# Optimization experiments

Hardware: AMD Instinct MI355X
Metric: run time of the kernel (lower is better)

Reference implementation:

```python
import jax, jax.numpy as jnp
import numpy as np

E = 8        # n_routed_experts
Z = 4        # zero_expert_num (identity experts)
K = 2        # moe_topk
SCALE = 2.5  # routed_scaling_factor
T, H, I = 8192, 1024, 512


def setup_inputs() -> dict:
    key = jax.random.key(0)
    k0, k1, k2, k3, k4 = jax.random.split(key, 5)
    return {
        "hidden_states": jax.random.normal(k0, (T, H), jnp.float32),
        "router_w": jax.random.normal(k1, (E + Z, H), jnp.float32) * 0.02,
        "correction_bias": jax.random.normal(k2, (E + Z,), jnp.float32) * 0.01,
        "w13": jax.random.normal(k3, (E, 2 * I, H), jnp.float32) * 0.02,
        "w2": jax.random.normal(k4, (E, H, I), jnp.float32) * 0.02,
    }


def reference(hidden_states, router_w, correction_bias, w13, w2):
    # ---- router (float32) ----
    logits = hidden_states.astype(jnp.float32) @ router_w.T          # [T, E+Z]
    scores = jax.nn.softmax(logits, axis=-1)
    # correction bias only affects expert *selection*, not the gate weights
    _, topk_idx = jax.lax.top_k(scores + correction_bias, K)          # [T, K]
    topk_w = jnp.take_along_axis(scores, topk_idx, axis=-1)          # renormalize=False

    # ---- zero experts (identity type): idx >= E contributes scale * x ----
    is_zero = topk_idx >= E                                           # [T, K]
    routed_w = jnp.where(is_zero, 0.0, topk_w)
    zero_scale = jnp.where(is_zero, topk_w, 0.0).sum(-1, keepdims=True)
    zero_result = zero_scale * hidden_states                          # [T, H]

    # ---- combine weights per routed expert: [T, E] ----
    tok = jnp.arange(hidden_states.shape[0])[:, None]
    safe_idx = jnp.clip(topk_idx, 0, E - 1)   # zero-expert slots carry weight 0
    combine = jnp.zeros((hidden_states.shape[0], E), scores.dtype)
    combine = combine.at[tok, safe_idx].add(routed_w)

    # ---- grouped expert GEMMs (SiLU gated MLP), combined densely ----
    h = jnp.einsum('th,eih->eti', hidden_states, w13)                 # [E, T, 2I]
    g, u = jnp.split(h, 2, axis=-1)
    act = jax.nn.silu(g) * u                                          # [E, T, I]
    eo = jnp.einsum('eti,ehi->eth', act, w2)                          # [E, T, H]
    routed = jnp.einsum('te,eth->th', combine, eo)                    # [T, H]

    return routed * SCALE + zero_result
```

## Files before the change

kernel.cpp:

```cpp
#include <hip/hip_runtime.h>
#include <hip/hip_bf16.h>
#include <math.h>

typedef __bf16 bf16_t;
typedef bf16_t bf16x8 __attribute__((ext_vector_type(8)));
typedef float f32x4 __attribute__((ext_vector_type(4)));

#define T_TOK 8192
#define HDIM  1024
#define IDIM  512
#define NEXP  8
#define NTOT  12
#define MAXROWS (2 * T_TOK + NEXP * 128)
#define MAX_MTILES (MAXROWS / 128)

__device__ __forceinline__ void gll16(const bf16_t* g, bf16_t* l) {
  __builtin_amdgcn_global_load_lds((__attribute__((address_space(1))) void*)g,
                                   (__attribute__((address_space(3))) void*)l,
                                   16, 0, 0);
}

__global__ void cast_bf16_kernel(const float* __restrict__ in, bf16_t* __restrict__ out,
                                 size_t n8) {
  size_t gid = (size_t)blockIdx.x * blockDim.x + threadIdx.x;
  if (gid >= n8) return;
  size_t i = gid * 8;
  float4 a = *(const float4*)&in[i];
  float4 b = *(const float4*)&in[i + 4];
  bf16x8 o;
  o[0] = (bf16_t)a.x; o[1] = (bf16_t)a.y; o[2] = (bf16_t)a.z; o[3] = (bf16_t)a.w;
  o[4] = (bf16_t)b.x; o[5] = (bf16_t)b.y; o[6] = (bf16_t)b.z; o[7] = (bf16_t)b.w;
  *(bf16x8*)&out[i] = o;
}

__global__ void router_kernel(const float* __restrict__ x, const float* __restrict__ rw,
                              const float* __restrict__ bias,
                              int* __restrict__ tk_e, float* __restrict__ tk_w,
                              float* __restrict__ zscale) {
  int t = blockIdx.x;
  int l = threadIdx.x;
  const float4* xr = (const float4*)(x + (size_t)t * HDIM);
  float4 xv[4];
#pragma unroll
  for (int i = 0; i < 4; i++) xv[i] = xr[l + 64 * i];
  float part[NTOT];
#pragma unroll
  for (int e = 0; e < NTOT; e++) {
    const float4* wr = (const float4*)(rw + (size_t)e * HDIM);
    float s = 0.f;
#pragma unroll
    for (int i = 0; i < 4; i++) {
      float4 w = wr[l + 64 * i];
      s += xv[i].x * w.x + xv[i].y * w.y + xv[i].z * w.z + xv[i].w * w.w;
    }
    part[e] = s;
  }
#pragma unroll
  for (int off = 32; off > 0; off >>= 1)
#pragma unroll
    for (int e = 0; e < NTOT; e++) part[e] += __shfl_down(part[e], off);

  if (l == 0) {
    float mx = part[0];
#pragma unroll
    for (int e = 1; e < NTOT; e++) mx = fmaxf(mx, part[e]);
    float p[NTOT], den = 0.f;
#pragma unroll
    for (int e = 0; e < NTOT; e++) { p[e] = expf(part[e] - mx); den += p[e]; }
    float inv = 1.f / den;
#pragma unroll
    for (int e = 0; e < NTOT; e++) p[e] *= inv;
    float s0 = -1e30f, s1 = -1e30f; int i0 = 0, i1 = 0;
#pragma unroll
    for (int e = 0; e < NTOT; e++) {
      float v = p[e] + bias[e];
      if (v > s0) { s1 = s0; i1 = i0; s0 = v; i0 = e; }
      else if (v > s1) { s1 = v; i1 = e; }
    }
    float zs = 0.f;
    int idx[2] = { i0, i1 };
#pragma unroll
    for (int k = 0; k < 2; k++) {
      int e = idx[k];
      float w = p[e];
      if (e >= NEXP) { zs += w; tk_e[2 * t + k] = -1; tk_w[2 * t + k] = 0.f; }
      else           { tk_e[2 * t + k] = e; tk_w[2 * t + k] = w; }
    }
    zscale[t] = zs;
  }
}

__global__ void zero_init_kernel(int* __restrict__ counts, int* __restrict__ sel_tok,
                                 float* __restrict__ sel_w) {
  int i = blockIdx.x * blockDim.x + threadIdx.x;
  if (i < MAXROWS) { sel_tok[i] = 0; sel_w[i] = 0.f; }
  if (i < NEXP) counts[i] = 0;
}

__global__ void count_kernel(const int* __restrict__ tk_e, int* __restrict__ counts) {
  __shared__ int lc[NEXP];
  int tid = threadIdx.x;
  if (tid < NEXP) lc[tid] = 0;
  __syncthreads();
  int t = blockIdx.x * blockDim.x + tid;
  int e0 = tk_e[2 * t], e1 = tk_e[2 * t + 1];
  if (e0 >= 0) atomicAdd(&lc[e0], 1);
  if (e1 >= 0) atomicAdd(&lc[e1], 1);
  __syncthreads();
  if (tid < NEXP) atomicAdd(&counts[tid], lc[tid]);
}

__global__ void scan_kernel(const int* __restrict__ counts, int* __restrict__ off_pad,
                            int* __restrict__ cursor, int* __restrict__ total_rows,
                            int* __restrict__ tile_e, int* __restrict__ tile_p0,
                            int* __restrict__ n_mtiles) {
  if (threadIdx.x == 0) {
    int run = 0, nt = 0;
    for (int e = 0; e < NEXP; e++) {
      off_pad[e] = run;
      cursor[e] = run;
      int ntile = (counts[e] + 127) / 128;
      for (int i = 0; i < ntile; i++) {
        tile_e[nt] = e;
        tile_p0[nt] = run + i * 128;
        nt++;
      }
      run += ntile * 128;
    }
    *total_rows = run;
    *n_mtiles = nt;
  }
}

__global__ void assign_kernel(const int* __restrict__ tk_e, const float* __restrict__ tk_w,
                              int* __restrict__ cursor, int* __restrict__ sel_tok,
                              float* __restrict__ sel_w, int* __restrict__ pos) {
  __shared__ int lc[NEXP];
  __shared__ int lbase[NEXP];
  int tid = threadIdx.x;
  if (tid < NEXP) lc[tid] = 0;
  __syncthreads();
  int t = blockIdx.x * blockDim.x + tid;
  int e0 = tk_e[2 * t], e1 = tk_e[2 * t + 1];
  int r0 = (e0 >= 0) ? atomicAdd(&lc[e0], 1) : -1;
  int r1 = (e1 >= 0) ? atomicAdd(&lc[e1], 1) : -1;
  __syncthreads();
  if (tid < NEXP) lbase[tid] = atomicAdd(&cursor[tid], lc[tid]);
  __syncthreads();
  int p0 = -1, p1 = -1;
  if (e0 >= 0) { p0 = lbase[e0] + r0; sel_tok[p0] = t; sel_w[p0] = 2.5f * tk_w[2 * t]; }
  if (e1 >= 0) { p1 = lbase[e1] + r1; sel_tok[p1] = t; sel_w[p1] = 2.5f * tk_w[2 * t + 1]; }
  pos[2 * t] = p0;
  pos[2 * t + 1] = p1;
}

__global__ void gather_cast_kernel(const float* __restrict__ x, const int* __restrict__ sel_tok,
                                   const int* __restrict__ total_rows, bf16_t* __restrict__ xg) {
  size_t gid = (size_t)blockIdx.x * blockDim.x + threadIdx.x;
  size_t p = gid >> 7;
  if (p >= (size_t)*total_rows) return;
  size_t j = (gid & 127) << 3;
  int t = sel_tok[p];
  float4 a = *(const float4*)&x[(size_t)t * HDIM + j];
  float4 b = *(const float4*)&x[(size_t)t * HDIM + j + 4];
  bf16x8 o;
  o[0] = (bf16_t)a.x; o[1] = (bf16_t)a.y; o[2] = (bf16_t)a.z; o[3] = (bf16_t)a.w;
  o[4] = (bf16_t)b.x; o[5] = (bf16_t)b.y; o[6] = (bf16_t)b.z; o[7] = (bf16_t)b.w;
  *(bf16x8*)&xg[p * HDIM + j] = o;
}

__global__ __launch_bounds__(256) void gemm1_kernel(
    const bf16_t* __restrict__ xg, const bf16_t* __restrict__ w13b,
    const int* __restrict__ tile_e, const int* __restrict__ tile_p0,
    const int* __restrict__ n_mtiles, bf16_t* __restrict__ actb) {
  const int ti = blockIdx.x;
  if (ti >= *n_mtiles) return;
  const int e = tile_e[ti];
  const int p0 = tile_p0[ti];
  const int g0 = blockIdx.y * 64;

  __shared__ alignas(16) bf16_t As[128 * 32];
  __shared__ alignas(16) bf16_t Bs[128 * 32];
  const int tid = threadIdx.x;
  const int w = tid >> 6, l = tid & 63;
  const int wr = w >> 1, wc = w & 1;
  const int quad = l >> 4, c16 = l & 15;

  const int sr = w * 32 + (l >> 2);
  const int sc = (l & 3) * 8;
  const bf16_t* Ag0 = xg + (size_t)(p0 + sr) * HDIM + sc;
  const bf16_t* w13e = w13b + (size_t)e * (2 * IDIM) * HDIM;
  int r0 = sr, r1 = sr + 16;
  int col0 = g0 + (r0 >> 6) * 32 + (((r0 >> 4) & 1) * 16) + (r0 & 15) + (((r0 >> 5) & 1) ? IDIM : 0);
  int col1 = g0 + (r1 >> 6) * 32 + (((r1 >> 4) & 1) * 16) + (r1 & 15) + (((r1 >> 5) & 1) ? IDIM : 0);
  const bf16_t* Bg0 = w13e + (size_t)col0 * HDIM + sc;
  const bf16_t* Bg1 = w13e + (size_t)col1 * HDIM + sc;
  bf16_t* Al0 = &As[(w * 32) * 32];
  bf16_t* Bl0 = &Bs[(w * 32) * 32];

  f32x4 acc[4][4];
#pragma unroll
  for (int i = 0; i < 4; i++)
#pragma unroll
    for (int j = 0; j < 4; j++) acc[i][j] = (f32x4){0.f, 0.f, 0.f, 0.f};

  for (int k0 = 0; k0 < HDIM; k0 += 32) {
    gll16(Ag0 + k0, Al0);
    gll16(Ag0 + k0 + (size_t)16 * HDIM, Al0 + 16 * 32);
    gll16(Bg0 + k0, Bl0);
    gll16(Bg1 + k0, Bl0 + 16 * 32);
    __syncthreads();
    bf16x8 af[4], bfv[4];
#pragma unroll
    for (int mt = 0; mt < 4; mt++)
      af[mt] = *(const bf16x8*)&As[(wr * 64 + mt * 16 + c16) * 32 + quad * 8];
#pragma unroll
    for (int nt = 0; nt < 4; nt++)
      bfv[nt] = *(const bf16x8*)&Bs[(wc * 64 + nt * 16 + c16) * 32 + quad * 8];
#pragma unroll
    for (int mt = 0; mt < 4; mt++)
#pragma unroll
      for (int nt = 0; nt < 4; nt++)
        acc[mt][nt] = __builtin_amdgcn_mfma_f32_16x16x32_bf16(af[mt], bfv[nt], acc[mt][nt], 0, 0, 0);
    __syncthreads();
  }

#pragma unroll
  for (int mt = 0; mt < 4; mt++) {
    int rowb = p0 + wr * 64 + mt * 16 + quad * 4;
#pragma unroll
    for (int nt = 0; nt < 2; nt++) {
      int col = g0 + wc * 32 + nt * 16 + c16;
#pragma unroll
      for (int r = 0; r < 4; r++) {
        float g = acc[mt][nt][r];
        float u = acc[mt][nt + 2][r];
        float s = g / (1.f + expf(-g));
        actb[(size_t)(rowb + r) * IDIM + col] = (bf16_t)(s * u);
      }
    }
  }
}

__global__ __launch_bounds__(256) void gemm2_kernel(
    const bf16_t* __restrict__ actb, const bf16_t* __restrict__ w2b,
    const float* __restrict__ sel_w, const int* __restrict__ tile_e,
    const int* __restrict__ tile_p0, const int* __restrict__ n_mtiles,
    bf16_t* __restrict__ eob) {
  const int ti = blockIdx.x;
  if (ti >= *n_mtiles) return;
  const int e = tile_e[ti];
  const int p0 = tile_p0[ti];
  const int n0 = blockIdx.y * 128;

  __shared__ alignas(16) bf16_t As[128 * 32];
  __shared__ alignas(16) bf16_t Bs[128 * 32];
  const int tid = threadIdx.x;
  const int w = tid >> 6, l = tid & 63;
  const int wr = w >> 1, wc = w & 1;
  const int quad = l >> 4, c16 = l & 15;

  const int sr = w * 32 + (l >> 2);
  const int sc = (l & 3) * 8;
  const bf16_t* Ag0 = actb + (size_t)(p0 + sr) * IDIM + sc;
  const bf16_t* Bg0 = w2b + (size_t)e * HDIM * IDIM + (size_t)(n0 + sr) * IDIM + sc;
  bf16_t* Al0 = &As[(w * 32) * 32];
  bf16_t* Bl0 = &Bs[(w * 32) * 32];

  f32x4 acc[4][4];
#pragma unroll
  for (int i = 0; i < 4; i++)
#pragma unroll
    for (int j = 0; j < 4; j++) acc[i][j] = (f32x4){0.f, 0.f, 0.f, 0.f};

  for (int k0 = 0; k0 < IDIM; k0 += 32) {
    gll16(Ag0 + k0, Al0);
    gll16(Ag0 + k0 + (size_t)16 * IDIM, Al0 + 16 * 32);
    gll16(Bg0 + k0, Bl0);
    gll16(Bg0 + k0 + (size_t)16 * IDIM, Bl0 + 16 * 32);
    __syncthreads();
    bf16x8 af[4], bfv[4];
#pragma unroll
    for (int mt = 0; mt < 4; mt++)
      af[mt] = *(const bf16x8*)&As[(wr * 64 + mt * 16 + c16) * 32 + quad * 8];
#pragma unroll
    for (int nt = 0; nt < 4; nt++)
      bfv[nt] = *(const bf16x8*)&Bs[(wc * 64 + nt * 16 + c16) * 32 + quad * 8];
#pragma unroll
    for (int mt = 0; mt < 4; mt++)
#pragma unroll
      for (int nt = 0; nt < 4; nt++)
        acc[mt][nt] = __builtin_amdgcn_mfma_f32_16x16x32_bf16(af[mt], bfv[nt], acc[mt][nt], 0, 0, 0);
    __syncthreads();
  }

#pragma unroll
  for (int mt = 0; mt < 4; mt++) {
    int rowb = wr * 64 + mt * 16 + quad * 4;
    float cw[4];
#pragma unroll
    for (int r = 0; r < 4; r++) cw[r] = sel_w[p0 + rowb + r];
#pragma unroll
    for (int nt = 0; nt < 4; nt++) {
      int col = n0 + wc * 64 + nt * 16 + c16;
#pragma unroll
      for (int r = 0; r < 4; r++)
        eob[(size_t)(p0 + rowb + r) * HDIM + col] = (bf16_t)(cw[r] * acc[mt][nt][r]);
    }
  }
}

__global__ void combine_kernel(const float* __restrict__ x, const float* __restrict__ zscale,
                               const int* __restrict__ pos, const bf16_t* __restrict__ eob,
                               float* __restrict__ out) {
  size_t gid = (size_t)blockIdx.x * blockDim.x + threadIdx.x;
  size_t t = gid >> 7;
  size_t j = (gid & 127) << 3;
  float zs = zscale[t];
  int p0 = pos[2 * t], p1 = pos[2 * t + 1];
  float4 a = *(const float4*)&x[t * HDIM + j];
  float4 b = *(const float4*)&x[t * HDIM + j + 4];
  float o[8] = { zs * a.x, zs * a.y, zs * a.z, zs * a.w,
                 zs * b.x, zs * b.y, zs * b.z, zs * b.w };
  if (p0 >= 0) {
    bf16x8 v = *(const bf16x8*)&eob[(size_t)p0 * HDIM + j];
#pragma unroll
    for (int k = 0; k < 8; k++) o[k] += (float)v[k];
  }
  if (p1 >= 0) {
    bf16x8 v = *(const bf16x8*)&eob[(size_t)p1 * HDIM + j];
#pragma unroll
    for (int k = 0; k < 8; k++) o[k] += (float)v[k];
  }
  *(float4*)&out[t * HDIM + j] = make_float4(o[0], o[1], o[2], o[3]);
  *(float4*)&out[t * HDIM + j + 4] = make_float4(o[4], o[5], o[6], o[7]);
}

extern "C" void kernel_launch(void* const* d_in, const int* in_sizes, int n_in,
                              void* d_out, int out_size, void* d_ws, size_t ws_size,
                              hipStream_t stream) {
  const float* x    = (const float*)d_in[0];
  const float* rw   = (const float*)d_in[1];
  const float* bias = (const float*)d_in[2];
  const float* w13  = (const float*)d_in[3];
  const float* w2   = (const float*)d_in[4];
  float* out = (float*)d_out;

  char* ws = (char*)d_ws;
  bf16_t* w13b = (bf16_t*)ws;  ws += (size_t)NEXP * 2 * IDIM * HDIM * 2;
  bf16_t* w2b  = (bf16_t*)ws;  ws += (size_t)NEXP * HDIM * IDIM * 2;
  bf16_t* xg   = (bf16_t*)ws;  ws += (size_t)MAXROWS * HDIM * 2;
  bf16_t* actb = (bf16_t*)ws;  ws += (size_t)MAXROWS * IDIM * 2;
  bf16_t* eob  = (bf16_t*)ws;  ws += (size_t)MAXROWS * HDIM * 2;
  int*   tk_e    = (int*)ws;   ws += (size_t)T_TOK * 2 * 4;
  float* tk_w    = (float*)ws; ws += (size_t)T_TOK * 2 * 4;
  float* zscale  = (float*)ws; ws += (size_t)T_TOK * 4;
  int*   pos     = (int*)ws;   ws += (size_t)T_TOK * 2 * 4;
  int*   sel_tok = (int*)ws;   ws += (size_t)MAXROWS * 4;
  float* sel_w   = (float*)ws; ws += (size_t)MAXROWS * 4;
  int*   counts  = (int*)ws;   ws += NEXP * 4;
  int*   off_pad = (int*)ws;   ws += NEXP * 4;
  int*   cursor  = (int*)ws;   ws += NEXP * 4;
  int*   total_rows = (int*)ws; ws += 4;
  int*   tile_e  = (int*)ws;   ws += MAX_MTILES * 4;
  int*   tile_p0 = (int*)ws;   ws += MAX_MTILES * 4;
  int*   n_mtiles = (int*)ws;  ws += 4;

  {
    size_t n8 = (size_t)NEXP * 2 * IDIM * HDIM / 8;
    cast_bf16_kernel<<<(n8 + 255) / 256, 256, 0, stream>>>(w13, w13b, n8);
    n8 = (size_t)NEXP * HDIM * IDIM / 8;
    cast_bf16_kernel<<<(n8 + 255) / 256, 256, 0, stream>>>(w2, w2b, n8);
  }
  router_kernel<<<T_TOK, 64, 0, stream>>>(x, rw, bias, tk_e, tk_w, zscale);
  zero_init_kernel<<<(MAXROWS + 255) / 256, 256, 0, stream>>>(counts, sel_tok, sel_w);
  count_kernel<<<T_TOK / 256, 256, 0, stream>>>(tk_e, counts);
  scan_kernel<<<1, 64, 0, stream>>>(counts, off_pad, cursor, total_rows,
                                    tile_e, tile_p0, n_mtiles);
  assign_kernel<<<T_TOK / 256, 256, 0, stream>>>(tk_e, tk_w, cursor, sel_tok, sel_w, pos);
  gather_cast_kernel<<<(size_t)MAXROWS * (HDIM / 8) / 256, 256, 0, stream>>>(
      x, sel_tok, total_rows, xg);

  gemm1_kernel<<<dim3(MAX_MTILES, IDIM / 64), 256, 0, stream>>>(
      xg, w13b, tile_e, tile_p0, n_mtiles, actb);
  gemm2_kernel<<<dim3(MAX_MTILES, HDIM / 128), 256, 0, stream>>>(
      actb, w2b, sel_w, tile_e, tile_p0, n_mtiles, eob);

  combine_kernel<<<(size_t)T_TOK * HDIM / 8 / 256, 256, 0, stream>>>(
      x, zscale, pos, eob, out);
}
```

Baseline: 235.9 us.

## Fuse MoE pipeline stages and scatter expert outputs via atomics into output

```diff
diff --git a/kernel.cpp b/kernel.cpp
--- a/kernel.cpp
+++ b/kernel.cpp
@@ -3,6 +3,7 @@
 #include <math.h>
 
 typedef __bf16 bf16_t;
+typedef bf16_t bf16x4 __attribute__((ext_vector_type(4)));
 typedef bf16_t bf16x8 __attribute__((ext_vector_type(8)));
 typedef float f32x4 __attribute__((ext_vector_type(4)));
 
@@ -20,25 +21,37 @@
                                    16, 0, 0);
 }
 
-__global__ void cast_bf16_kernel(const float* __restrict__ in, bf16_t* __restrict__ out,
-                                 size_t n8) {
+#define N1G (NEXP * 2 * IDIM * HDIM / 8)
+#define N2G (NEXP * HDIM * IDIM / 8)
+__global__ void cast_w_kernel(const float* __restrict__ w13, const float* __restrict__ w2,
+                              bf16_t* __restrict__ w13b, bf16_t* __restrict__ w2b) {
   size_t gid = (size_t)blockIdx.x * blockDim.x + threadIdx.x;
-  if (gid >= n8) return;
-  size_t i = gid * 8;
-  float4 a = *(const float4*)&in[i];
-  float4 b = *(const float4*)&in[i + 4];
+  const float* src;
+  bf16_t* dst;
+  if (gid < N1G) { src = w13 + gid * 8; dst = w13b + gid * 8; }
+  else { size_t g2 = gid - N1G; if (g2 >= N2G) return; src = w2 + g2 * 8; dst = w2b + g2 * 8; }
+  float4 a = *(const float4*)src;
+  float4 b = *(const float4*)(src + 4);
   bf16x8 o;
   o[0] = (bf16_t)a.x; o[1] = (bf16_t)a.y; o[2] = (bf16_t)a.z; o[3] = (bf16_t)a.w;
   o[4] = (bf16_t)b.x; o[5] = (bf16_t)b.y; o[6] = (bf16_t)b.z; o[7] = (bf16_t)b.w;
-  *(bf16x8*)&out[i] = o;
+  *(bf16x8*)dst = o;
+}
+
+__global__ void zero_counts_kernel(int* __restrict__ counts) {
+  if (threadIdx.x < NEXP) counts[threadIdx.x] = 0;
 }
 
 __global__ void router_kernel(const float* __restrict__ x, const float* __restrict__ rw,
                               const float* __restrict__ bias,
                               int* __restrict__ tk_e, float* __restrict__ tk_w,
-                              float* __restrict__ zscale) {
-  int t = blockIdx.x;
-  int l = threadIdx.x;
+                              float* __restrict__ zscale, int* __restrict__ counts) {
+  __shared__ int lc[NEXP];
+  int tid = threadIdx.x;
+  if (tid < NEXP) lc[tid] = 0;
+  __syncthreads();
+  int t = blockIdx.x * 4 + (tid >> 6);
+  int l = tid & 63;
   const float4* xr = (const float4*)(x + (size_t)t * HDIM);
   float4 xv[4];
 #pragma unroll
@@ -84,119 +97,115 @@
       int e = idx[k];
       float w = p[e];
       if (e >= NEXP) { zs += w; tk_e[2 * t + k] = -1; tk_w[2 * t + k] = 0.f; }
-      else           { tk_e[2 * t + k] = e; tk_w[2 * t + k] = w; }
+      else { tk_e[2 * t + k] = e; tk_w[2 * t + k] = w; atomicAdd(&lc[e], 1); }
     }
     zscale[t] = zs;
   }
-}
-
-__global__ void zero_init_kernel(int* __restrict__ counts, int* __restrict__ sel_tok,
-                                 float* __restrict__ sel_w) {
-  int i = blockIdx.x * blockDim.x + threadIdx.x;
-  if (i < MAXROWS) { sel_tok[i] = 0; sel_w[i] = 0.f; }
-  if (i < NEXP) counts[i] = 0;
-}
-
-__global__ void count_kernel(const int* __restrict__ tk_e, int* __restrict__ counts) {
-  __shared__ int lc[NEXP];
-  int tid = threadIdx.x;
-  if (tid < NEXP) lc[tid] = 0;
-  __syncthreads();
-  int t = blockIdx.x * blockDim.x + tid;
-  int e0 = tk_e[2 * t], e1 = tk_e[2 * t + 1];
-  if (e0 >= 0) atomicAdd(&lc[e0], 1);
-  if (e1 >= 0) atomicAdd(&lc[e1], 1);
-  __syncthreads();
-  if (tid < NEXP) atomicAdd(&counts[tid], lc[tid]);
-}
-
-__global__ void scan_kernel(const int* __restrict__ counts, int* __restrict__ off_pad,
-                            int* __restrict__ cursor, int* __restrict__ total_rows,
+  __syncthreads();
+  if (tid < NEXP && lc[tid]) atomicAdd(&counts[tid], lc[tid]);
+}
+
+__global__ void scan_kernel(const int* __restrict__ counts, int* __restrict__ cursor,
                             int* __restrict__ tile_e, int* __restrict__ tile_p0,
-                            int* __restrict__ n_mtiles) {
+                            int* __restrict__ n_mtiles,
+                            int* __restrict__ sel_tok, float* __restrict__ sel_w) {
+  __shared__ int s_off[NEXP], s_cnt[NEXP];
   if (threadIdx.x == 0) {
     int run = 0, nt = 0;
     for (int e = 0; e < NEXP; e++) {
-      off_pad[e] = run;
+      s_off[e] = run; s_cnt[e] = counts[e];
       cursor[e] = run;
-      int ntile = (counts[e] + 127) / 128;
-      for (int i = 0; i < ntile; i++) {
-        tile_e[nt] = e;
-        tile_p0[nt] = run + i * 128;
-        nt++;
-      }
+      int ntile = (s_cnt[e] + 127) / 128;
+      for (int i = 0; i < ntile; i++) { tile_e[nt] = e; tile_p0[nt] = run + i * 128; nt++; }
       run += ntile * 128;
     }
-    *total_rows = run;
     *n_mtiles = nt;
   }
-}
-
-__global__ void assign_kernel(const int* __restrict__ tk_e, const float* __restrict__ tk_w,
-                              int* __restrict__ cursor, int* __restrict__ sel_tok,
-                              float* __restrict__ sel_w, int* __restrict__ pos) {
-  __shared__ int lc[NEXP];
-  __shared__ int lbase[NEXP];
+  __syncthreads();
+  for (int i = threadIdx.x; i < NEXP * 128; i += blockDim.x) {
+    int e = i >> 7, idx = i & 127;
+    int c = s_cnt[e];
+    int padded = ((c + 127) / 128) * 128;
+    int pos = c + idx;
+    if (pos < padded) { sel_tok[s_off[e] + pos] = 0; sel_w[s_off[e] + pos] = 0.f; }
+  }
+}
+
+__global__ __launch_bounds__(256) void assign_gather_kernel(
+    const float* __restrict__ x, const int* __restrict__ tk_e, const float* __restrict__ tk_w,
+    const float* __restrict__ zscale, int* __restrict__ cursor,
+    int* __restrict__ sel_tok, float* __restrict__ sel_w,
+    bf16_t* __restrict__ xg, float* __restrict__ out) {
+  __shared__ int lc[NEXP], lbase[NEXP];
+  __shared__ int s_p0[256], s_p1[256];
+  __shared__ float s_zs[256];
   int tid = threadIdx.x;
+  int t = blockIdx.x * 256 + tid;
   if (tid < NEXP) lc[tid] = 0;
   __syncthreads();
-  int t = blockIdx.x * blockDim.x + tid;
   int e0 = tk_e[2 * t], e1 = tk_e[2 * t + 1];
   int r0 = (e0 >= 0) ? atomicAdd(&lc[e0], 1) : -1;
   int r1 = (e1 >= 0) ? atomicAdd(&lc[e1], 1) : -1;
   __syncthreads();
-  if (tid < NEXP) lbase[tid] = atomicAdd(&cursor[tid], lc[tid]);
+  if (tid < NEXP) lbase[tid] = lc[tid] ? atomicAdd(&cursor[tid], lc[tid]) : 0;
   __syncthreads();
   int p0 = -1, p1 = -1;
   if (e0 >= 0) { p0 = lbase[e0] + r0; sel_tok[p0] = t; sel_w[p0] = 2.5f * tk_w[2 * t]; }
   if (e1 >= 0) { p1 = lbase[e1] + r1; sel_tok[p1] = t; sel_w[p1] = 2.5f * tk_w[2 * t + 1]; }
-  pos[2 * t] = p0;
-  pos[2 * t + 1] = p1;
-}
-
-__global__ void gather_cast_kernel(const float* __restrict__ x, const int* __restrict__ sel_tok,
-                                   const int* __restrict__ total_rows, bf16_t* __restrict__ xg) {
-  size_t gid = (size_t)blockIdx.x * blockDim.x + threadIdx.x;
-  size_t p = gid >> 7;
-  if (p >= (size_t)*total_rows) return;
-  size_t j = (gid & 127) << 3;
-  int t = sel_tok[p];
-  float4 a = *(const float4*)&x[(size_t)t * HDIM + j];
-  float4 b = *(const float4*)&x[(size_t)t * HDIM + j + 4];
-  bf16x8 o;
-  o[0] = (bf16_t)a.x; o[1] = (bf16_t)a.y; o[2] = (bf16_t)a.z; o[3] = (bf16_t)a.w;
-  o[4] = (bf16_t)b.x; o[5] = (bf16_t)b.y; o[6] = (bf16_t)b.z; o[7] = (bf16_t)b.w;
-  *(bf16x8*)&xg[p * HDIM + j] = o;
+  s_p0[tid] = p0; s_p1[tid] = p1; s_zs[tid] = zscale[t];
+  __syncthreads();
+
+  size_t tbase = (size_t)blockIdx.x * 256;
+  int j = tid * 4;
+  for (int i = 0; i < 256; i++) {
+    float4 v = *(const float4*)&x[(tbase + i) * HDIM + j];
+    float zs = s_zs[i];
+    *(float4*)&out[(tbase + i) * HDIM + j] = make_float4(zs * v.x, zs * v.y, zs * v.z, zs * v.w);
+    bf16x4 b;
+    b[0] = (bf16_t)v.x; b[1] = (bf16_t)v.y; b[2] = (bf16_t)v.z; b[3] = (bf16_t)v.w;
+    int q0 = s_p0[i], q1 = s_p1[i];
+    if (q0 >= 0) *(bf16x4*)&xg[(size_t)q0 * HDIM + j] = b;
+    if (q1 >= 0) *(bf16x4*)&xg[(size_t)q1 * HDIM + j] = b;
+  }
 }
 
 __global__ __launch_bounds__(256) void gemm1_kernel(
     const bf16_t* __restrict__ xg, const bf16_t* __restrict__ w13b,
     const int* __restrict__ tile_e, const int* __restrict__ tile_p0,
     const int* __restrict__ n_mtiles, bf16_t* __restrict__ actb) {
-  const int ti = blockIdx.x;
+  const int yb = blockIdx.x & 7;
+  const int ti = blockIdx.x >> 3;
   if (ti >= *n_mtiles) return;
   const int e = tile_e[ti];
   const int p0 = tile_p0[ti];
-  const int g0 = blockIdx.y * 64;
-
-  __shared__ alignas(16) bf16_t As[128 * 32];
-  __shared__ alignas(16) bf16_t Bs[128 * 32];
+  const int g0 = yb * 64;
+
+  __shared__ alignas(16) bf16_t As[4096];
+  __shared__ alignas(16) bf16_t Bs[4096];
+
   const int tid = threadIdx.x;
   const int w = tid >> 6, l = tid & 63;
   const int wr = w >> 1, wc = w & 1;
   const int quad = l >> 4, c16 = l & 15;
 
-  const int sr = w * 32 + (l >> 2);
-  const int sc = (l & 3) * 8;
-  const bf16_t* Ag0 = xg + (size_t)(p0 + sr) * HDIM + sc;
+  const bf16_t* Asrc0 = xg + (size_t)(p0 + l) * HDIM + w * 8;
+  const bf16_t* Asrc1 = Asrc0 + (size_t)64 * HDIM;
+  int rB0 = l, rB1 = l + 64;
+  int col0 = g0 + (rB0 >> 6) * 32 + (((rB0 >> 4) & 1) * 16) + (rB0 & 15) + (((rB0 >> 5) & 1) ? IDIM : 0);
+  int col1 = g0 + (rB1 >> 6) * 32 + (((rB1 >> 4) & 1) * 16) + (rB1 & 15) + (((rB1 >> 5) & 1) ? IDIM : 0);
   const bf16_t* w13e = w13b + (size_t)e * (2 * IDIM) * HDIM;
-  int r0 = sr, r1 = sr + 16;
-  int col0 = g0 + (r0 >> 6) * 32 + (((r0 >> 4) & 1) * 16) + (r0 & 15) + (((r0 >> 5) & 1) ? IDIM : 0);
-  int col1 = g0 + (r1 >> 6) * 32 + (((r1 >> 4) & 1) * 16) + (r1 & 15) + (((r1 >> 5) & 1) ? IDIM : 0);
-  const bf16_t* Bg0 = w13e + (size_t)col0 * HDIM + sc;
-  const bf16_t* Bg1 = w13e + (size_t)col1 * HDIM + sc;
-  bf16_t* Al0 = &As[(w * 32) * 32];
-  bf16_t* Bl0 = &Bs[(w * 32) * 32];
+  const bf16_t* Bsrc0 = w13e + (size_t)col0 * HDIM + w * 8;
+  const bf16_t* Bsrc1 = w13e + (size_t)col1 * HDIM + w * 8;
+  bf16_t* Adst0 = &As[w * 1024];
+  bf16_t* Adst1 = &As[w * 1024 + 512];
+  bf16_t* Bdst0 = &Bs[w * 1024];
+  bf16_t* Bdst1 = &Bs[w * 1024 + 512];
+
+  int aoff[4], boff[4];
+#pragma unroll
+  for (int mt = 0; mt < 4; mt++) aoff[mt] = quad * 1024 + (wr * 64 + mt * 16 + c16) * 8;
+#pragma unroll
+  for (int nt = 0; nt < 4; nt++) boff[nt] = quad * 1024 + (wc * 64 + nt * 16 + c16) * 8;
 
   f32x4 acc[4][4];
 #pragma unroll
@@ -205,18 +214,16 @@
     for (int j = 0; j < 4; j++) acc[i][j] = (f32x4){0.f, 0.f, 0.f, 0.f};
 
   for (int k0 = 0; k0 < HDIM; k0 += 32) {
-    gll16(Ag0 + k0, Al0);
-    gll16(Ag0 + k0 + (size_t)16 * HDIM, Al0 + 16 * 32);
-    gll16(Bg0 + k0, Bl0);
-    gll16(Bg1 + k0, Bl0 + 16 * 32);
+    gll16(Asrc0 + k0, Adst0);
+    gll16(Asrc1 + k0, Adst1);
+    gll16(Bsrc0 + k0, Bdst0);
+    gll16(Bsrc1 + k0, Bdst1);
     __syncthreads();
     bf16x8 af[4], bfv[4];
 #pragma unroll
-    for (int mt = 0; mt < 4; mt++)
-      af[mt] = *(const bf16x8*)&As[(wr * 64 + mt * 16 + c16) * 32 + quad * 8];
-#pragma unroll
-    for (int nt = 0; nt < 4; nt++)
-      bfv[nt] = *(const bf16x8*)&Bs[(wc * 64 + nt * 16 + c16) * 32 + quad * 8];
+    for (int mt = 0; mt < 4; mt++) af[mt] = *(const bf16x8*)&As[aoff[mt]];
+#pragma unroll
+    for (int nt = 0; nt < 4; nt++) bfv[nt] = *(const bf16x8*)&Bs[boff[nt]];
 #pragma unroll
     for (int mt = 0; mt < 4; mt++)
 #pragma unroll
@@ -235,8 +242,7 @@
       for (int r = 0; r < 4; r++) {
         float g = acc[mt][nt][r];
         float u = acc[mt][nt + 2][r];
-        float s = g / (1.f + expf(-g));
-        actb[(size_t)(rowb + r) * IDIM + col] = (bf16_t)(s * u);
+        actb[(size_t)(rowb + r) * IDIM + col] = (bf16_t)(g / (1.f + expf(-g)) * u);
       }
     }
   }
@@ -244,28 +250,39 @@
 
 __global__ __launch_bounds__(256) void gemm2_kernel(
     const bf16_t* __restrict__ actb, const bf16_t* __restrict__ w2b,
-    const float* __restrict__ sel_w, const int* __restrict__ tile_e,
-    const int* __restrict__ tile_p0, const int* __restrict__ n_mtiles,
-    bf16_t* __restrict__ eob) {
-  const int ti = blockIdx.x;
+    const float* __restrict__ sel_w, const int* __restrict__ sel_tok,
+    const int* __restrict__ tile_e, const int* __restrict__ tile_p0,
+    const int* __restrict__ n_mtiles, float* __restrict__ out) {
+  const int yb = blockIdx.x & 7;
+  const int ti = blockIdx.x >> 3;
   if (ti >= *n_mtiles) return;
   const int e = tile_e[ti];
   const int p0 = tile_p0[ti];
-  const int n0 = blockIdx.y * 128;
-
-  __shared__ alignas(16) bf16_t As[128 * 32];
-  __shared__ alignas(16) bf16_t Bs[128 * 32];
+  const int n0 = yb * 128;
+
+  __shared__ alignas(16) bf16_t As[4096];
+  __shared__ alignas(16) bf16_t Bs[4096];
+
   const int tid = threadIdx.x;
   const int w = tid >> 6, l = tid & 63;
   const int wr = w >> 1, wc = w & 1;
   const int quad = l >> 4, c16 = l & 15;
 
-  const int sr = w * 32 + (l >> 2);
-  const int sc = (l & 3) * 8;
-  const bf16_t* Ag0 = actb + (size_t)(p0 + sr) * IDIM + sc;
-  const bf16_t* Bg0 = w2b + (size_t)e * HDIM * IDIM + (size_t)(n0 + sr) * IDIM + sc;
-  bf16_t* Al0 = &As[(w * 32) * 32];
-  bf16_t* Bl0 = &Bs[(w * 32) * 32];
+  const bf16_t* Asrc0 = actb + (size_t)(p0 + l) * IDIM + w * 8;
+  const bf16_t* Asrc1 = Asrc0 + (size_t)64 * IDIM;
+  const bf16_t* w2e = w2b + (size_t)e * HDIM * IDIM;
+  const bf16_t* Bsrc0 = w2e + (size_t)(n0 + l) * IDIM + w * 8;
+  const bf16_t* Bsrc1 = Bsrc0 + (size_t)64 * IDIM;
+  bf16_t* Adst0 = &As[w * 1024];
+  bf16_t* Adst1 = &As[w * 1024 + 512];
+  bf16_t* Bdst0 = &Bs[w * 1024];
+  bf16_t* Bdst1 = &Bs[w * 1024 + 512];
+
+  int aoff[4], boff[4];
+#pragma unroll
+  for (int mt = 0; mt < 4; mt++) aoff[mt] = quad * 1024 + (wr * 64 + mt * 16 + c16) * 8;
+#pragma unroll
+  for (int nt = 0; nt < 4; nt++) boff[nt] = quad * 1024 + (wc * 64 + nt * 16 + c16) * 8;
 
   f32x4 acc[4][4];
 #pragma unroll
@@ -274,18 +291,16 @@
     for (int j = 0; j < 4; j++) acc[i][j] = (f32x4){0.f, 0.f, 0.f, 0.f};
 
   for (int k0 = 0; k0 < IDIM; k0 += 32) {
-    gll16(Ag0 + k0, Al0);
-    gll16(Ag0 + k0 + (size_t)16 * IDIM, Al0 + 16 * 32);
-    gll16(Bg0 + k0, Bl0);
-    gll16(Bg0 + k0 + (size_t)16 * IDIM, Bl0 + 16 * 32);
+    gll16(Asrc0 + k0, Adst0);
+    gll16(Asrc1 + k0, Adst1);
+    gll16(Bsrc0 + k0, Bdst0);
+    gll16(Bsrc1 + k0, Bdst1);
     __syncthreads();
     bf16x8 af[4], bfv[4];
 #pragma unroll
-    for (int mt = 0; mt < 4; mt++)
-      af[mt] = *(const bf16x8*)&As[(wr * 64 + mt * 16 + c16) * 32 + quad * 8];
-#pragma unroll
-    for (int nt = 0; nt < 4; nt++)
-      bfv[nt] = *(const bf16x8*)&Bs[(wc * 64 + nt * 16 + c16) * 32 + quad * 8];
+    for (int mt = 0; mt < 4; mt++) af[mt] = *(const bf16x8*)&As[aoff[mt]];
+#pragma unroll
+    for (int nt = 0; nt < 4; nt++) bfv[nt] = *(const bf16x8*)&Bs[boff[nt]];
 #pragma unroll
     for (int mt = 0; mt < 4; mt++)
 #pragma unroll
@@ -296,44 +311,20 @@
 
 #pragma unroll
   for (int mt = 0; mt < 4; mt++) {
-    int rowb = wr * 64 + mt * 16 + quad * 4;
-    float cw[4];
-#pragma unroll
-    for (int r = 0; r < 4; r++) cw[r] = sel_w[p0 + rowb + r];
-#pragma unroll
-    for (int nt = 0; nt < 4; nt++) {
-      int col = n0 + wc * 64 + nt * 16 + c16;
-#pragma unroll
-      for (int r = 0; r < 4; r++)
-        eob[(size_t)(p0 + rowb + r) * HDIM + col] = (bf16_t)(cw[r] * acc[mt][nt][r]);
-    }
-  }
-}
-
-__global__ void combine_kernel(const float* __restrict__ x, const float* __restrict__ zscale,
-                               const int* __restrict__ pos, const bf16_t* __restrict__ eob,
-                               float* __restrict__ out) {
-  size_t gid = (size_t)blockIdx.x * blockDim.x + threadIdx.x;
-  size_t t = gid >> 7;
-  size_t j = (gid & 127) << 3;
-  float zs = zscale[t];
-  int p0 = pos[2 * t], p1 = pos[2 * t + 1];
-  float4 a = *(const float4*)&x[t * HDIM + j];
-  float4 b = *(const float4*)&x[t * HDIM + j + 4];
-  float o[8] = { zs * a.x, zs * a.y, zs * a.z, zs * a.w,
-                 zs * b.x, zs * b.y, zs * b.z, zs * b.w };
-  if (p0 >= 0) {
-    bf16x8 v = *(const bf16x8*)&eob[(size_t)p0 * HDIM + j];
-#pragma unroll
-    for (int k = 0; k < 8; k++) o[k] += (float)v[k];
-  }
-  if (p1 >= 0) {
-    bf16x8 v = *(const bf16x8*)&eob[(size_t)p1 * HDIM + j];
-#pragma unroll
-    for (int k = 0; k < 8; k++) o[k] += (float)v[k];
-  }
-  *(float4*)&out[t * HDIM + j] = make_float4(o[0], o[1], o[2], o[3]);
-  *(float4*)&out[t * HDIM + j + 4] = make_float4(o[4], o[5], o[6], o[7]);
+    int rowb = p0 + wr * 64 + mt * 16 + quad * 4;
+#pragma unroll
+    for (int r = 0; r < 4; r++) {
+      int p = rowb + r;
+      float cw = sel_w[p];
+      if (cw == 0.f) continue;
+      size_t obase = (size_t)sel_tok[p] * HDIM;
+#pragma unroll
+      for (int nt = 0; nt < 4; nt++) {
+        int col = n0 + wc * 64 + nt * 16 + c16;
+        atomicAdd(&out[obase + col], cw * acc[mt][nt][r]);
+      }
+    }
+  }
 }
 
 extern "C" void kernel_launch(void* const* d_in, const int* in_sizes, int n_in,
@@ -351,41 +342,26 @@
   bf16_t* w2b  = (bf16_t*)ws;  ws += (size_t)NEXP * HDIM * IDIM * 2;
   bf16_t* xg   = (bf16_t*)ws;  ws += (size_t)MAXROWS * HDIM * 2;
   bf16_t* actb = (bf16_t*)ws;  ws += (size_t)MAXROWS * IDIM * 2;
-  bf16_t* eob  = (bf16_t*)ws;  ws += (size_t)MAXROWS * HDIM * 2;
   int*   tk_e    = (int*)ws;   ws += (size_t)T_TOK * 2 * 4;
   float* tk_w    = (float*)ws; ws += (size_t)T_TOK * 2 * 4;
   float* zscale  = (float*)ws; ws += (size_t)T_TOK * 4;
-  int*   pos     = (int*)ws;   ws += (size_t)T_TOK * 2 * 4;
   int*   sel_tok = (int*)ws;   ws += (size_t)MAXROWS * 4;
   float* sel_w   = (float*)ws; ws += (size_t)MAXROWS * 4;
   int*   counts  = (int*)ws;   ws += NEXP * 4;
-  int*   off_pad = (int*)ws;   ws += NEXP * 4;
   int*   cursor  = (int*)ws;   ws += NEXP * 4;
-  int*   total_rows = (int*)ws; ws += 4;
   int*   tile_e  = (int*)ws;   ws += MAX_MTILES * 4;
   int*   tile_p0 = (int*)ws;   ws += MAX_MTILES * 4;
   int*   n_mtiles = (int*)ws;  ws += 4;
 
-  {
-    size_t n8 = (size_t)NEXP * 2 * IDIM * HDIM / 8;
-    cast_bf16_kernel<<<(n8 + 255) / 256, 256, 0, stream>>>(w13, w13b, n8);
-    n8 = (size_t)NEXP * HDIM * IDIM / 8;
-    cast_bf16_kernel<<<(n8 + 255) / 256, 256, 0, stream>>>(w2, w2b, n8);
-  }
-  router_kernel<<<T_TOK, 64, 0, stream>>>(x, rw, bias, tk_e, tk_w, zscale);
-  zero_init_kernel<<<(MAXROWS + 255) / 256, 256, 0, stream>>>(counts, sel_tok, sel_w);
-  count_kernel<<<T_TOK / 256, 256, 0, stream>>>(tk_e, counts);
-  scan_kernel<<<1, 64, 0, stream>>>(counts, off_pad, cursor, total_rows,
-                                    tile_e, tile_p0, n_mtiles);
-  assign_kernel<<<T_TOK / 256, 256, 0, stream>>>(tk_e, tk_w, cursor, sel_tok, sel_w, pos);
-  gather_cast_kernel<<<(size_t)MAXROWS * (HDIM / 8) / 256, 256, 0, stream>>>(
-      x, sel_tok, total_rows, xg);
-
-  gemm1_kernel<<<dim3(MAX_MTILES, IDIM / 64), 256, 0, stream>>>(
+  zero_counts_kernel<<<1, 64, 0, stream>>>(counts);
+  cast_w_kernel<<<(N1G + N2G + 255) / 256, 256, 0, stream>>>(w13, w2, w13b, w2b);
+  router_kernel<<<T_TOK / 4, 256, 0, stream>>>(x, rw, bias, tk_e, tk_w, zscale, counts);
+  scan_kernel<<<1, 256, 0, stream>>>(counts, cursor, tile_e, tile_p0, n_mtiles, sel_tok, sel_w);
+  assign_gather_kernel<<<T_TOK / 256, 256, 0, stream>>>(
+      x, tk_e, tk_w, zscale, cursor, sel_tok, sel_w, xg, out);
+
+  gemm1_kernel<<<MAX_MTILES * 8, 256, 0, stream>>>(
       xg, w13b, tile_e, tile_p0, n_mtiles, actb);
-  gemm2_kernel<<<dim3(MAX_MTILES, HDIM / 128), 256, 0, stream>>>(
-      actb, w2b, sel_w, tile_e, tile_p0, n_mtiles, eob);
-
-  combine_kernel<<<(size_t)T_TOK * HDIM / 8 / 256, 256, 0, stream>>>(
-      x, zscale, pos, eob, out);
-}
+  gemm2_kernel<<<MAX_MTILES * 8, 256, 0, stream>>>(
+      actb, w2b, sel_w, sel_tok, tile_e, tile_p0, n_mtiles, out);
+}
```

Result: slower. 353.6 us (+49.9%).
